# Optimization experiments

Hardware: AMD Instinct MI355X
Metric: run time of the kernel (lower is better)

The kernel has to match this reference:

```python
import jax, jax.numpy as jnp
import numpy as np
from jax import lax

K = 8            # number of object slots
H = 250          # hidden / fc_size
EPS = 1e-5
DN = ('NCHW', 'OIHW', 'NCHW')


def ln_all(x):
    # F.layer_norm over all non-batch dims, no affine params (torch init: w=1,b=0)
    ax = tuple(range(1, x.ndim))
    m = jnp.mean(x, ax, keepdims=True)
    v = jnp.var(x, ax, keepdims=True)
    return (x - m) * lax.rsqrt(v + EPS)


def ln_last(x):
    # nn.LayerNorm(feat) -> last dim only
    m = jnp.mean(x, -1, keepdims=True)
    v = jnp.var(x, -1, keepdims=True)
    return (x - m) * lax.rsqrt(v + EPS)


def conv(x, w, b):
    # torch Conv2d(k=4, s=2, p=1), NCHW
    y = lax.conv_general_dilated(x, w, (2, 2), [(1, 1), (1, 1)], dimension_numbers=DN)
    return y + b[None, :, None, None]


def up4(x):
    return jnp.repeat(jnp.repeat(x, 4, axis=2), 4, axis=3)


def setup_inputs():
    ks = jax.random.split(jax.random.key(0), 20)
    bk = 48 * K
    p = lambda i, shape, s: jax.random.normal(ks[i], shape, jnp.float32) * s
    z = lambda n: jnp.zeros((n,), jnp.float32)
    return dict(
        x=p(0, (bk, 4096), 1.0),
        state=p(1, (bk, H), 1.0),
        # encoder convs (OIHW) + fc
        c1w=p(2, (16, 1, 4, 4), 0.25), c1b=z(16),
        c2w=p(3, (32, 16, 4, 4), 0.06), c2b=z(32),
        c3w=p(4, (64, 32, 4, 4), 0.04), c3b=z(64),
        efc_w=p(5, (4096, 512), 0.016), efc_b=z(512),
        # R_NEM (weights stored as [in, out])
        renc_w=p(6, (H, H), 0.06), renc_b=z(H),
        core_w=p(7, (2 * H, H), 0.045), core_b=z(H),
        ctx_w=p(8, (H, H), 0.06), ctx_b=z(H),
        att1_w=p(9, (H, 100), 0.06), att1_b=z(100),
        att2_w=p(10, (100, 1), 0.1), att2_b=z(1),
        out_w=p(11, (2 * H + 512, H), 0.03), out_b=z(H),
        # decoder fcs + convs
        dfc1_w=p(12, (H, 512), 0.06), dfc1_b=z(512),
        dfc2_w=p(13, (512, 4096), 0.045), dfc2_b=z(4096),
        d1w=p(14, (32, 64, 4, 4), 0.03), d1b=z(32),
        d2w=p(15, (16, 32, 4, 4), 0.045), d2b=z(16),
        d3w=p(16, (1, 16, 4, 4), 0.06), d3b=z(1),
    )


def reference(x, state, c1w, c1b, c2w, c2b, c3w, c3b, efc_w, efc_b,
              renc_w, renc_b, core_w, core_b, ctx_w, ctx_b,
              att1_w, att1_b, att2_w, att2_b, out_w, out_b,
              dfc1_w, dfc1_b, dfc2_w, dfc2_b, d1w, d1b, d2w, d2b, d3w, d3b):
    bk = x.shape[0]
    b = bk // K

    # ---------------- EncoderLayer ----------------
    def inwrap(h, w, bias):  # InputWrapper conv branch: NHWC -> permute(0,3,2,1) -> conv -> back
        y = conv(jnp.transpose(h, (0, 3, 2, 1)), w, bias)
        return jax.nn.elu(ln_all(jnp.transpose(y, (0, 3, 2, 1))))

    h = x.reshape(bk, 64, 64, 1)
    h = inwrap(h, c1w, c1b)                 # (bk,32,32,16)
    h = inwrap(h, c2w, c2b)                 # (bk,16,16,32)
    h = inwrap(h, c3w, c3b)                 # (bk,8,8,64)
    h = h.reshape(bk, -1)                   # (bk,4096)
    h = jax.nn.elu(ln_last(h @ efc_w + efc_b))   # (bk,512)

    # ---------------- R_NEM (RecurrentLayer) ----------------
    s1 = jax.nn.relu(ln_last(state @ renc_w + renc_b))   # (bk,H)
    s1r = s1.reshape(b, K, H)
    idx = np.array([[j for j in range(K) if j != i] for i in range(K)])  # (K,K-1)
    cs = s1r[:, idx, :]                                    # context: (b,K,K-1,H)
    fs = jnp.broadcast_to(s1r[:, :, None, :], cs.shape)    # focus copies
    pair = jnp.concatenate([fs, cs], axis=-1)              # (b,K,K-1,2H)
    core = jax.nn.relu(ln_last(pair @ core_w + core_b))    # (b,K,K-1,H)
    ctx = jax.nn.relu(ln_last(core @ ctx_w + ctx_b))       # (b,K,K-1,H)
    att = jax.nn.sigmoid(jnp.tanh(ln_last(core @ att1_w + att1_b)) @ att2_w + att2_b)  # (b,K,K-1,1)
    effect = jnp.sum(ctx * att, axis=2).reshape(bk, H)     # attention-weighted sum over K-1
    total = jnp.concatenate([s1, effect, h], axis=1)       # (bk, 2H+512)
    new_state = total @ out_w + out_b                      # (bk,H)
    xr = jax.nn.sigmoid(ln_last(new_state))
    state_out = jax.nn.sigmoid(new_state)

    # ---------------- DecoderLayer ----------------
    d = jax.nn.relu(ln_last(xr @ dfc1_w + dfc1_b))         # (bk,512)
    d = jax.nn.relu(ln_last(d @ dfc2_w + dfc2_b))          # (bk,4096)
    d = d.reshape(bk, 8, 8, 64)

    def outwrap(t, w, bias):
        y = conv(up4(jnp.transpose(t, (0, 3, 2, 1))), w, bias)
        return jnp.transpose(y, (0, 3, 2, 1))

    d = jax.nn.relu(ln_all(outwrap(d, d1w, d1b)))          # (bk,16,16,32)
    d = jax.nn.relu(ln_all(outwrap(d, d2w, d2b)))          # (bk,32,32,16)
    d = jax.nn.sigmoid(outwrap(d, d3w, d3b))               # (bk,64,64,1), no LN
    x_out = d.reshape(bk, -1)                              # (bk,4096)
    return x_out, state_out
```

## Files before the change

kernel.cpp:

```cpp
#include <hip/hip_runtime.h>
#include <hip/hip_bf16.h>
#include <math.h>

#define ST_ENC2 0
#define ST_ENC3 1
#define ST_DEC1 2
#define ST_DEC2 3
#define ST_ENC1 4

typedef __attribute__((ext_vector_type(8))) short bf16x8;
typedef __attribute__((ext_vector_type(4))) float f32x4;

__device__ __forceinline__ float eluf(float v){ return v > 0.f ? v : expm1f(v); }
__device__ __forceinline__ float sigf(float v){ return 1.f/(1.f+expf(-v)); }
__device__ __forceinline__ unsigned short f2bf(float f){
  unsigned u = __float_as_uint(f);
  u += 0x7FFFu + ((u >> 16) & 1u);
  return (unsigned short)(u >> 16);
}
__device__ __forceinline__ float bf2f(short s){
  return __uint_as_float(((unsigned)(unsigned short)s) << 16);
}

__device__ __forceinline__ void block_reduce2(float& a, float& b, float* sbuf){
  __syncthreads();
  for (int off = 32; off; off >>= 1){
    a += __shfl_down(a, off);
    b += __shfl_down(b, off);
  }
  int lane = threadIdx.x & 63, w = threadIdx.x >> 6;
  if (lane == 0){ sbuf[2*w] = a; sbuf[2*w+1] = b; }
  __syncthreads();
  if (threadIdx.x == 0){
    int nw = blockDim.x >> 6;
    float sa = 0.f, sb = 0.f;
    for (int i = 0; i < nw; i++){ sa += sbuf[2*i]; sb += sbuf[2*i+1]; }
    sbuf[0] = sa; sbuf[1] = sb;
  }
  __syncthreads();
  a = sbuf[0]; b = sbuf[1];
}

__device__ __forceinline__ float fold_sum(const float* __restrict__ w, int O, int I,
                                          int o, int i, int pa, int pb, int da, int db){
  float s = 0.f;
  for (int kh = 0; kh < 4; kh++){
    bool inh = (pb==0) ? (db==0 ? (kh==0) : (kh>=1)) : (db==0 ? (kh<=2) : (kh==3));
    if (!inh) continue;
    for (int kw = 0; kw < 4; kw++){
      bool inw = (pa==0) ? (da==0 ? (kw==0) : (kw>=1)) : (da==0 ? (kw<=2) : (kw==3));
      if (!inw) continue;
      s += w[((o*I + i)*4 + kh)*4 + kw];
    }
  }
  return s;
}
__device__ __forceinline__ void fold_elem(const float* __restrict__ w, float* __restrict__ CW,
                                          int O, int I, int l){
  int o = l % O; int q = l / O;
  int da = q & 1, db = (q>>1)&1, pa = (q>>2)&1, pb = (q>>3)&1, i = q>>4;
  CW[(((pb*2+pa)*4 + db*2+da)*I + i)*O + o] = fold_sum(w, O, I, o, i, pa, pb, da, db);
}
__device__ __forceinline__ void cvtc2_elem(const float* __restrict__ w, short* __restrict__ D, int l){
  int i = l & 15, t = (l>>4) & 15, o = l>>8;
  D[l] = (short)f2bf(w[(o*16 + i)*16 + t]);
}
__device__ __forceinline__ void cvtc3_elem(const float* __restrict__ w, short* __restrict__ D, int l){
  int i = l & 31, t = (l>>5) & 15, o = l>>9;
  D[l] = (short)f2bf(w[(o*32 + i)*16 + t]);
}
__device__ __forceinline__ void foldd1_elem(const float* __restrict__ w, short* __restrict__ D, int l){
  int i = l & 63, tap = (l>>6)&3, o = (l>>8)&31, ph = l>>13;
  D[l] = (short)f2bf(fold_sum(w, 32, 64, o, i, ph&1, ph>>1, tap&1, tap>>1));
}
__device__ __forceinline__ void foldd2_elem(const float* __restrict__ w, short* __restrict__ D, int l){
  int i = l & 31, tap = (l>>5)&3, o = (l>>7)&15, ph = l>>11;
  D[l] = (short)f2bf(fold_sum(w, 16, 32, o, i, ph&1, ph>>1, tap&1, tap>>1));
}

__global__ __launch_bounds__(256) void prep_all(
  float* __restrict__ stat,
  const float* __restrict__ d3w, float* __restrict__ CWT3,
  const float* __restrict__ c2w, short* __restrict__ BtC2,
  const float* __restrict__ c3w, short* __restrict__ BtC3,
  const float* __restrict__ d1w, short* __restrict__ BD1,
  const float* __restrict__ d2w, short* __restrict__ BD2,
  const float* __restrict__ state, short* __restrict__ SBF)
{
  const int S0=3840, F3=S0+256, P2=F3+8192, P3=P2+32768, P4=P3+32768, P5=P4+8192,
            TOTAL=P5+98304;
  for (int l = blockIdx.x*blockDim.x + threadIdx.x; l < TOTAL; l += gridDim.x*blockDim.x){
    if (l < S0)      stat[l] = 0.f;
    else if (l < F3) fold_elem(d3w, CWT3, 1, 16, l - S0);
    else if (l < P2) cvtc2_elem(c2w, BtC2, l - F3);
    else if (l < P3) cvtc3_elem(c3w, BtC3, l - P2);
    else if (l < P4) foldd1_elem(d1w, BD1, l - P3);
    else if (l < P5) foldd2_elem(d2w, BD2, l - P4);
    else {
      int q = l - P5;
      int n = q >> 8, k = q & 255;
      SBF[q] = (k < 250) ? (short)f2bf(state[n*250 + k]) : (short)0;
    }
  }
}

__global__ __launch_bounds__(256) void transpose_cvt_all(
  const float* __restrict__ efc,  short* __restrict__ Defc,
  const float* __restrict__ dfc2, short* __restrict__ Ddfc2,
  const float* __restrict__ outw, short* __restrict__ Dout,
  const float* __restrict__ corew,short* __restrict__ Dcore,
  const float* __restrict__ dfc1, short* __restrict__ Ddfc1,
  const float* __restrict__ renc, short* __restrict__ Drenc,
  const float* __restrict__ ctx,  short* __restrict__ Dctx,
  const float* __restrict__ att1, short* __restrict__ Datt1)
{
  int bx = blockIdx.x;
  const float* W; short* D; int K, N, Kp, base;
  if      (bx < 512) { W=efc;  D=Defc;  K=4096; N=512;  Kp=4096; base=0;    }
  else if (bx < 1024){ W=dfc2; D=Ddfc2; K=512;  N=4096; Kp=512;  base=512;  }
  else if (bx < 1088){ W=outw; D=Dout;  K=1012; N=250;  Kp=1024; base=1024; }
  else if (bx < 1120){ W=corew;D=Dcore; K=500;  N=250;  Kp=512;  base=1088; }
  else if (bx < 1152){ W=dfc1; D=Ddfc1; K=250;  N=512;  Kp=256;  base=1120; }
  else if (bx < 1168){ W=renc; D=Drenc; K=250;  N=250;  Kp=256;  base=1152; }
  else if (bx < 1184){ W=ctx;  D=Dctx;  K=250;  N=250;  Kp=256;  base=1168; }
  else               { W=att1; D=Datt1; K=250;  N=100;  Kp=256;  base=1184; }
  int t = bx - base;
  int tpr = Kp >> 6;
  int tk = t % tpr, tn = t / tpr;
  __shared__ short tile[64][65];
  int c = threadIdx.x & 63, r4 = threadIdx.x >> 6;
  int n0 = tn*64, k0 = tk*64;
  #pragma unroll 4
  for (int p = 0; p < 16; p++){
    int r = r4*16 + p;
    int k = k0 + r, n = n0 + c;
    float v = (k < K && n < N) ? W[(size_t)k*N + n] : 0.f;
    tile[c][r] = (short)f2bf(v);
  }
  __syncthreads();
  #pragma unroll 4
  for (int p = 0; p < 16; p++){
    int nn = r4*16 + p;
    int n = n0 + nn;
    if (n < N) D[(size_t)n*Kp + k0 + c] = tile[nn][c];
  }
}

__global__ __launch_bounds__(256) void cvt_ln_elu(
    const short* __restrict__ inb, const float* __restrict__ stat, short* __restrict__ outb)
{
  int n = blockIdx.x, tid = threadIdx.x;
  float sm = stat[n*2], sq = stat[n*2+1];
  float m = sm*(1.f/4096.f), rs = rsqrtf(sq*(1.f/4096.f) - m*m + 1e-5f);
  const short* ip = inb + (size_t)n*4096;
  short* op = outb + (size_t)n*4096;
  for (int l = tid*4; l < 4096; l += 1024){
    uint2 rv = *(const uint2*)&ip[l];
    float v0 = bf2f((short)(rv.x & 0xFFFF)), v1 = bf2f((short)(rv.x >> 16));
    float v2 = bf2f((short)(rv.y & 0xFFFF)), v3 = bf2f((short)(rv.y >> 16));
    uint2 pk;
    pk.x = f2bf(eluf((v0-m)*rs)) | ((unsigned)f2bf(eluf((v1-m)*rs))<<16);
    pk.y = f2bf(eluf((v2-m)*rs)) | ((unsigned)f2bf(eluf((v3-m)*rs))<<16);
    *(uint2*)&op[l] = pk;
  }
}

__global__ __launch_bounds__(256) void gemm_mfma(
    const short* __restrict__ Ab, const short* __restrict__ Bt,
    float* __restrict__ P, int M, int N, int Kp, int Kc)
{
  __shared__ __align__(16) short As[64*32];
  __shared__ __align__(16) short Bs[64*32];
  int tid = threadIdx.x;
  int bm = blockIdx.y*64, bn = blockIdx.x*64;
  int kb = blockIdx.z * Kc;
  int kend = kb + Kc;

  int r = tid >> 2, c = tid & 3;
  const short* Arow = Ab + (size_t)(bm + r)*Kp;
  int gn = bn + r;
  bool bval = gn < N;
  const short* Brow = Bt + (size_t)gn*Kp;

  uint4 hA, hB;
  auto load_regs = [&](int k0){
    hA = *(const uint4*)&Arow[k0 + c*8];
    hB = bval ? *(const uint4*)&Brow[k0 + c*8] : make_uint4(0,0,0,0);
  };
  auto write_lds = [&](){
    *(uint4*)&As[r*32 + c*8] = hA;
    *(uint4*)&Bs[r*32 + c*8] = hB;
  };

  int wave = tid >> 6;
  int ln = tid & 15, quad = (tid >> 4) & 3;
  int wr = (wave >> 1) * 32, wc = (wave & 1) * 32;

  f32x4 zero = {0.f, 0.f, 0.f, 0.f};
  f32x4 acc[2][2] = {{zero, zero}, {zero, zero}};

  load_regs(kb);
  write_lds();
  __syncthreads();
  for (int k0 = kb; k0 < kend; k0 += 32){
    int nxt = k0 + 32;
    if (nxt < kend) load_regs(nxt);
    bf16x8 a0 = *(const bf16x8*)&As[(wr +      ln)*32 + quad*8];
    bf16x8 a1 = *(const bf16x8*)&As[(wr + 16 + ln)*32 + quad*8];
    bf16x8 b0 = *(const bf16x8*)&Bs[(wc +      ln)*32 + quad*8];
    bf16x8 b1 = *(const bf16x8*)&Bs[(wc + 16 + ln)*32 + quad*8];
    acc[0][0] = __builtin_amdgcn_mfma_f32_16x16x32_bf16(a0, b0, acc[0][0], 0, 0, 0);
    acc[0][1] = __builtin_amdgcn_mfma_f32_16x16x32_bf16(a0, b1, acc[0][1], 0, 0, 0);
    acc[1][0] = __builtin_amdgcn_mfma_f32_16x16x32_bf16(a1, b0, acc[1][0], 0, 0, 0);
    acc[1][1] = __builtin_amdgcn_mfma_f32_16x16x32_bf16(a1, b1, acc[1][1], 0, 0, 0);
    __syncthreads();
    if (nxt < kend){ write_lds(); __syncthreads(); }
  }

  float* Pout = P + (size_t)blockIdx.z*M*N;
  #pragma unroll
  for (int t = 0; t < 2; t++)
    #pragma unroll
    for (int u = 0; u < 2; u++)
      #pragma unroll
      for (int j = 0; j < 4; j++){
        int row = bm + wr + t*16 + quad*4 + j;
        int col = bn + wc + u*16 + ln;
        if (col < N) Pout[(size_t)row*N + col] = acc[t][u][j];
      }
}

__global__ __launch_bounds__(256) void reduce_ln(
    const float* __restrict__ Pp, const float* __restrict__ bias,
    void* __restrict__ outp, int M, int N, int KS, int os, int act, int obf)
{
  __shared__ float rowbuf[4096];
  __shared__ float sbuf[16];
  int row = blockIdx.x;
  size_t MN = (size_t)M*N;
  float s = 0.f, s2 = 0.f;
  for (int c = threadIdx.x; c < N; c += 256){
    float v = bias[c];
    for (int ks = 0; ks < KS; ks++) v += Pp[ks*MN + (size_t)row*N + c];
    rowbuf[c] = v; s += v; s2 += v*v;
  }
  block_reduce2(s, s2, sbuf);
  float m = s / N;
  float r = rsqrtf(s2/N - m*m + 1e-5f);
  for (int c = threadIdx.x; c < N; c += 256){
    float v = (rowbuf[c]-m)*r;
    if (act == 1) v = fmaxf(v, 0.f);
    else if (act == 2) v = eluf(v);
    else if (act == 3) v = tanhf(v);
    if (obf) ((short*)outp)[(size_t)row*os + c] = f2bf(v);
    else     ((float*)outp)[(size_t)row*os + c] = v;
  }
}

__global__ __launch_bounds__(256) void reduce_ns(
    const float* __restrict__ Pp, const float* __restrict__ bias,
    short* __restrict__ XRb, float* __restrict__ so, int M, int N, int KS)
{
  __shared__ float rowbuf[256];
  __shared__ float sbuf[16];
  int row = blockIdx.x;
  size_t MN = (size_t)M*N;
  float s = 0.f, s2 = 0.f;
  for (int c = threadIdx.x; c < N; c += 256){
    float v = bias[c];
    for (int ks = 0; ks < KS; ks++) v += Pp[ks*MN + (size_t)row*N + c];
    rowbuf[c] = v; s += v; s2 += v*v;
  }
  block_reduce2(s, s2, sbuf);
  float m = s / N;
  float r = rsqrtf(s2/N - m*m + 1e-5f);
  for (int c = threadIdx.x; c < N; c += 256){
    float v = rowbuf[c];
    XRb[(size_t)row*256 + c] = f2bf(sigf((v-m)*r));
    so[(size_t)row*N + c] = sigf(v);
  }
}

__global__ __launch_bounds__(256) void enc_conv1_ig(
    const float* __restrict__ x, const float* __restrict__ w, const float* __restrict__ bias,
    short* __restrict__ outp, float* __restrict__ stat)
{
  __shared__ __align__(16) float in_t[66*68];
  __shared__ float sbuf[16];
  int n = blockIdx.x, tid = threadIdx.x;
  for (int l = tid; l < 66*68; l += 256) in_t[l] = 0.f;
  __syncthreads();
  const float* xin = x + (size_t)n*4096;
  for (int l4 = tid; l4 < 1024; l4 += 256){
    float4 v = *(const float4*)&xin[l4*4];
    int aa = (l4*4) >> 6, bb = (l4*4) & 63;
    float* dst = &in_t[(aa+1)*68 + bb + 1];
    dst[0]=v.x; dst[1]=v.y; dst[2]=v.z; dst[3]=v.w;
  }
  int o = tid & 15;
  float wr[16];
  #pragma unroll
  for (int t = 0; t < 16; t++) wr[t] = w[o*16 + t];
  float bv = bias[o];
  __syncthreads();
  float s = 0.f, s2 = 0.f;
  short* op = outp + (size_t)n*16384;
  for (int r = 0; r < 64; r++){
    int idx = tid + (r<<8);
    int bq = (idx>>4)&31, aq = idx>>9;
    int a0 = 2*aq, b0 = 2*bq;
    float acc = bv;
    #pragma unroll
    for (int kw = 0; kw < 4; kw++){
      const float* row = &in_t[(a0+kw)*68 + b0];
      float2 p0 = *(const float2*)&row[0];
      float2 p1 = *(const float2*)&row[2];
      acc += p0.x*wr[0*4+kw] + p0.y*wr[1*4+kw] + p1.x*wr[2*4+kw] + p1.y*wr[3*4+kw];
    }
    op[idx] = f2bf(acc);
    s += acc; s2 += acc*acc;
  }
  block_reduce2(s, s2, sbuf);
  if (tid == 0){ atomicAdd(&stat[n*2], s); atomicAdd(&stat[n*2+1], s2); }
}

__global__ __launch_bounds__(256) void enc_conv2_mfma(
    const short* __restrict__ in, const short* __restrict__ Bt, const float* __restrict__ bias,
    const float* __restrict__ stat_in, short* __restrict__ outp, float* __restrict__ stat)
{
  __shared__ __align__(16) short in_t[34*34*16];
  __shared__ float sbuf[16];
  int n = blockIdx.x, tid = threadIdx.x;
  float smv = stat_in[n*2], sqv = stat_in[n*2+1];
  float m = smv*(1.f/16384.f), rs = rsqrtf(sqv*(1.f/16384.f) - m*m + 1e-5f);
  for (int l = tid; l < 34*34*16/4; l += 256) ((unsigned long long*)in_t)[l] = 0ull;
  __syncthreads();
  const short* ip = in + (size_t)n*16384;
  for (int l = tid; l < 4096; l += 256){
    int i4 = l & 3, bb = (l>>2) & 31, aa = l>>7;
    uint2 rv = *(const uint2*)&ip[aa*512 + bb*16 + i4*4];
    float v0 = bf2f((short)(rv.x & 0xFFFF)), v1 = bf2f((short)(rv.x >> 16));
    float v2 = bf2f((short)(rv.y & 0xFFFF)), v3 = bf2f((short)(rv.y >> 16));
    uint2 pk;
    pk.x = f2bf(eluf((v0-m)*rs)) | ((unsigned)f2bf(eluf((v1-m)*rs))<<16);
    pk.y = f2bf(eluf((v2-m)*rs)) | ((unsigned)f2bf(eluf((v3-m)*rs))<<16);
    *(uint2*)&in_t[((aa+1)*34 + (bb+1))*16 + i4*4] = pk;
  }
  int wave = tid>>6, ln = tid&15, quad = (tid>>4)&3;
  bf16x8 bfr[2][8];
  #pragma unroll
  for (int nt = 0; nt < 2; nt++){
    const short* Brow = Bt + (nt*16 + ln)*256;
    #pragma unroll
    for (int ks = 0; ks < 8; ks++)
      bfr[nt][ks] = *(const bf16x8*)&Brow[ks*32 + quad*8];
  }
  __syncthreads();
  f32x4 z = {0.f,0.f,0.f,0.f};
  f32x4 acc[2][4] = {{z,z,z,z},{z,z,z,z}};
  int tapq = quad>>1, io = (quad&1)*8;
  #pragma unroll
  for (int ks = 0; ks < 8; ks++){
    int t = 2*ks + tapq;
    int kh = t>>2, kw = t&3;
    #pragma unroll
    for (int mt = 0; mt < 4; mt++){
      int p = (wave*4 + mt)*16 + ln;
      int oa = p>>4, ob = p&15;
      bf16x8 a = *(const bf16x8*)&in_t[((2*oa+kw)*34 + (2*ob+kh))*16 + io];
      acc[0][mt] = __builtin_amdgcn_mfma_f32_16x16x32_bf16(a, bfr[0][ks], acc[0][mt],0,0,0);
      acc[1][mt] = __builtin_amdgcn_mfma_f32_16x16x32_bf16(a, bfr[1][ks], acc[1][mt],0,0,0);
    }
  }
  float s = 0.f, s2 = 0.f;
  short* op = outp + (size_t)n*8192;
  #pragma unroll
  for (int nt = 0; nt < 2; nt++){
    int o = nt*16 + ln;
    float bz = bias[o];
    #pragma unroll
    for (int mt = 0; mt < 4; mt++)
      #pragma unroll
      for (int j = 0; j < 4; j++){
        int p = (wave*4 + mt)*16 + quad*4 + j;
        float v = acc[nt][mt][j] + bz;
        s += v; s2 += v*v;
        int oa = p>>4, ob = p&15;
        op[oa*512 + ob*32 + o] = f2bf(v);
      }
  }
  block_reduce2(s, s2, sbuf);
  if (tid == 0){ atomicAdd(&stat[n*2], s); atomicAdd(&stat[n*2+1], s2); }
}

__global__ __launch_bounds__(256) void enc_conv3_mfma(
    const short* __restrict__ in, const short* __restrict__ Bt, const float* __restrict__ bias,
    const float* __restrict__ stat_in, short* __restrict__ outp, float* __restrict__ stat)
{
  __shared__ __align__(16) short in_t[18*18*32];
  __shared__ float sbuf[16];
  int n = blockIdx.x, tid = threadIdx.x;
  float smv = stat_in[n*2], sqv = stat_in[n*2+1];
  float m = smv*(1.f/8192.f), rs = rsqrtf(sqv*(1.f/8192.f) - m*m + 1e-5f);
  for (int l = tid; l < 18*18*32/4; l += 256) ((unsigned long long*)in_t)[l] = 0ull;
  __syncthreads();
  const short* ip = in + (size_t)n*8192;
  for (int l = tid; l < 2048; l += 256){
    int i4 = l & 7, bb = (l>>3)&15, aa = l>>7;
    uint2 rv = *(const uint2*)&ip[aa*512 + bb*32 + i4*4];
    float v0 = bf2f((short)(rv.x & 0xFFFF)), v1 = bf2f((short)(rv.x >> 16));
    float v2 = bf2f((short)(rv.y & 0xFFFF)), v3 = bf2f((short)(rv.y >> 16));
    uint2 pk;
    pk.x = f2bf(eluf((v0-m)*rs)) | ((unsigned)f2bf(eluf((v1-m)*rs))<<16);
    pk.y = f2bf(eluf((v2-m)*rs)) | ((unsigned)f2bf(eluf((v3-m)*rs))<<16);
    *(uint2*)&in_t[((aa+1)*18 + (bb+1))*32 + i4*4] = pk;
  }
  int wave = tid>>6, ln = tid&15, quad = (tid>>4)&3;
  int o = wave*16 + ln;
  bf16x8 bfr[16];
  {
    const short* Brow = Bt + o*512;
    #pragma unroll
    for (int ks = 0; ks < 16; ks++)
      bfr[ks] = *(const bf16x8*)&Brow[ks*32 + quad*8];
  }
  __syncthreads();
  f32x4 z = {0.f,0.f,0.f,0.f};
  f32x4 acc[4] = {z,z,z,z};
  #pragma unroll
  for (int ks = 0; ks < 16; ks++){
    int kh = ks>>2, kw = ks&3;
    #pragma unroll
    for (int mt = 0; mt < 4; mt++){
      int p = mt*16 + ln;
      int oa = p>>3, ob = p&7;
      bf16x8 a = *(const bf16x8*)&in_t[((2*oa+kw)*18 + (2*ob+kh))*32 + quad*8];
      acc[mt] = __builtin_amdgcn_mfma_f32_16x16x32_bf16(a, bfr[ks], acc[mt],0,0,0);
    }
  }
  float s = 0.f, s2 = 0.f;
  float bz = bias[o];
  short* op = outp + (size_t)n*4096;
  #pragma unroll
  for (int mt = 0; mt < 4; mt++)
    #pragma unroll
    for (int j = 0; j < 4; j++){
      int p = mt*16 + quad*4 + j;
      int oa = p>>3, ob = p&7;
      float v = acc[mt][j] + bz;
      s += v; s2 += v*v;
      op[oa*512 + ob*64 + o] = f2bf(v);
    }
  block_reduce2(s, s2, sbuf);
  if (tid == 0){ atomicAdd(&stat[n*2], s); atomicAdd(&stat[n*2+1], s2); }
}

__global__ __launch_bounds__(256) void dec_conv1_mfma(
    const short* __restrict__ in, const short* __restrict__ Bd, const float* __restrict__ bias,
    short* __restrict__ outp, float* __restrict__ stat)
{
  __shared__ __align__(16) short in_t[10*10*64];
  __shared__ float sbuf[16];
  int n = blockIdx.x, tid = threadIdx.x;
  for (int l = tid; l < 10*10*64/4; l += 256) ((unsigned long long*)in_t)[l] = 0ull;
  __syncthreads();
  const short* ip = in + (size_t)n*4096;
  for (int l = tid; l < 1024; l += 256){
    int i4 = l & 15, sb = (l>>4)&7, sa = l>>7;
    *(uint2*)&in_t[((sa+1)*10 + (sb+1))*64 + i4*4] = *(const uint2*)&ip[sa*512 + sb*64 + i4*4];
  }
  int wave = tid>>6, ln = tid&15, quad = (tid>>4)&3;
  int pa = wave & 1, pb = wave >> 1;
  bf16x8 bfr[2][8];
  #pragma unroll
  for (int nt = 0; nt < 2; nt++){
    const short* Brow = Bd + (wave*32 + nt*16 + ln)*256;
    #pragma unroll
    for (int ks = 0; ks < 8; ks++)
      bfr[nt][ks] = *(const bf16x8*)&Brow[ks*32 + quad*8];
  }
  __syncthreads();
  f32x4 z = {0.f,0.f,0.f,0.f};
  f32x4 acc[2][4] = {{z,z,z,z},{z,z,z,z}};
  #pragma unroll
  for (int ks = 0; ks < 8; ks++){
    int tap = ks>>1, ibase = (ks&1)*32 + quad*8;
    int da = tap & 1, db = tap >> 1;
    #pragma unroll
    for (int mt = 0; mt < 4; mt++){
      int p = mt*16 + ln;
      int ta = p>>3, tb = p&7;
      bf16x8 a = *(const bf16x8*)&in_t[((ta+da+pa)*10 + (tb+db+pb))*64 + ibase];
      acc[0][mt] = __builtin_amdgcn_mfma_f32_16x16x32_bf16(a, bfr[0][ks], acc[0][mt],0,0,0);
      acc[1][mt] = __builtin_amdgcn_mfma_f32_16x16x32_bf16(a, bfr[1][ks], acc[1][mt],0,0,0);
    }
  }
  float s = 0.f, s2 = 0.f;
  short* op = outp + (size_t)n*8192;
  #pragma unroll
  for (int nt = 0; nt < 2; nt++){
    int o = nt*16 + ln;
    float bz = bias[o];
    #pragma unroll
    for (int mt = 0; mt < 4; mt++)
      #pragma unroll
      for (int j = 0; j < 4; j++){
        int p = mt*16 + quad*4 + j;
        int ta = p>>3, tb = p&7;
        float v = acc[nt][mt][j] + bz;
        s += v; s2 += v*v;
        op[(2*ta+pa)*512 + (2*tb+pb)*32 + o] = f2bf(v);
      }
  }
  block_reduce2(s, s2, sbuf);
  if (tid == 0){ atomicAdd(&stat[n*2], s); atomicAdd(&stat[n*2+1], s2); }
}

__global__ __launch_bounds__(256) void dec_conv2_mfma(
    const short* __restrict__ in, const short* __restrict__ Bd, const float* __restrict__ bias,
    const float* __restrict__ stat_in, short* __restrict__ outp, float* __restrict__ stat)
{
  __shared__ __align__(16) short in_t[18*18*32];
  __shared__ float sbuf[16];
  int n = blockIdx.x, tid = threadIdx.x;
  float smv = stat_in[n*2], sqv = stat_in[n*2+1];
  float m = smv*(1.f/8192.f), rs = rsqrtf(sqv*(1.f/8192.f) - m*m + 1e-5f);
  for (int l = tid; l < 18*18*32/4; l += 256) ((unsigned long long*)in_t)[l] = 0ull;
  __syncthreads();
  const short* ip = in + (size_t)n*8192;
  for (int l = tid; l < 2048; l += 256){
    int i4 = l & 7, sb = (l>>3)&15, sa = l>>7;
    uint2 rv = *(const uint2*)&ip[sa*512 + sb*32 + i4*4];
    float v0 = bf2f((short)(rv.x & 0xFFFF)), v1 = bf2f((short)(rv.x >> 16));
    float v2 = bf2f((short)(rv.y & 0xFFFF)), v3 = bf2f((short)(rv.y >> 16));
    uint2 pk;
    pk.x = f2bf(fmaxf((v0-m)*rs,0.f)) | ((unsigned)f2bf(fmaxf((v1-m)*rs,0.f))<<16);
    pk.y = f2bf(fmaxf((v2-m)*rs,0.f)) | ((unsigned)f2bf(fmaxf((v3-m)*rs,0.f))<<16);
    *(uint2*)&in_t[((sa+1)*18 + (sb+1))*32 + i4*4] = pk;
  }
  int wave = tid>>6, ln = tid&15, quad = (tid>>4)&3;
  int pa = wave & 1, pb = wave >> 1;
  bf16x8 bfr[4];
  {
    const short* Brow = Bd + (wave*16 + ln)*128;
    #pragma unroll
    for (int ks = 0; ks < 4; ks++)
      bfr[ks] = *(const bf16x8*)&Brow[ks*32 + quad*8];
  }
  __syncthreads();
  f32x4 z = {0.f,0.f,0.f,0.f};
  f32x4 acc[16] = {z,z,z,z,z,z,z,z,z,z,z,z,z,z,z,z};
  #pragma unroll
  for (int ks = 0; ks < 4; ks++){
    int da = ks & 1, db = ks >> 1;
    #pragma unroll
    for (int mt = 0; mt < 16; mt++){
      int p = mt*16 + ln;
      int ta = p>>4, tb = p&15;
      bf16x8 a = *(const bf16x8*)&in_t[((ta+da+pa)*18 + (tb+db+pb))*32 + quad*8];
      acc[mt] = __builtin_amdgcn_mfma_f32_16x16x32_bf16(a, bfr[ks], acc[mt],0,0,0);
    }
  }
  float s = 0.f, s2 = 0.f;
  float bz = bias[ln];
  short* op = outp + (size_t)n*16384;
  #pragma unroll
  for (int mt = 0; mt < 16; mt++)
    #pragma unroll
    for (int j = 0; j < 4; j++){
      int p = mt*16 + quad*4 + j;
      int ta = p>>4, tb = p&15;
      float v = acc[mt][j] + bz;
      s += v; s2 += v*v;
      op[(2*ta+pa)*512 + (2*tb+pb)*16 + ln] = f2bf(v);
    }
  block_reduce2(s, s2, sbuf);
  if (tid == 0){ atomicAdd(&stat[n*2], s); atomicAdd(&stat[n*2+1], s2); }
}

__global__ __launch_bounds__(256) void dec_conv3_ig(
    const short* __restrict__ in, const float* __restrict__ CWT, const float* __restrict__ bias,
    const float* __restrict__ stat_in, float* __restrict__ outp)
{
  __shared__ __align__(16) float in_t[9792];
  __shared__ __align__(16) float wl[256];
  int bx = blockIdx.x;
  int n = bx >> 1, b0 = (bx & 1) * 32, tb0 = b0 >> 1;
  int tid = threadIdx.x;
  float sm = stat_in[n*2], sq = stat_in[n*2+1];
  float m = sm*(1.f/16384.f), rs = rsqrtf(sq*(1.f/16384.f) - m*m + 1e-5f);
  const short* ip = in + (size_t)n*16384;
  for (int l = tid; l < 9792; l += 256){
    int i = l & 15, sb = (l >> 4) % 18, sap = l / 288;
    int sa = sap - 1, sbg = tb0 - 1 + sb;
    float v = 0.f;
    if ((unsigned)sa < 32u && (unsigned)sbg < 32u)
      v = fmaxf((bf2f(ip[sa*512 + sbg*16 + i])-m)*rs, 0.f);
    in_t[(sap*18 + sb)*16 + i] = v;
  }
  for (int l = tid; l < 256; l += 256) wl[l] = CWT[l];
  __syncthreads();
  float bv = bias[0];
  int bl = tid & 31, ath = tid >> 5;
  int b = b0 + bl;
  int tb = b >> 1, pb = b & 1;
  float* op = outp + (size_t)n*4096;
  #pragma unroll
  for (int j = 0; j < 8; j++){
    int a = ath*8 + j;
    int ta = a >> 1, pa = a & 1;
    float4 s4 = make_float4(0.f,0.f,0.f,0.f);
    #pragma unroll
    for (int db = 0; db < 2; db++){
      int sb = tb + db + (pb ? 0 : -1);
      int sbl = sb - (tb0 - 1);
      #pragma unroll
      for (int da = 0; da < 2; da++){
        int sa = ta + da + (pa ? 0 : -1);
        int sap = sa + 1;
        const float4* A4 = (const float4*)&in_t[(sap*18 + sbl)*16];
        const float4* B4 = (const float4*)&wl[((pb*2+pa)*4 + db*2+da)*16];
        #pragma unroll
        for (int q = 0; q < 4; q++){
          float4 av = A4[q], bw = B4[q];
          s4.x += av.x*bw.x; s4.y += av.y*bw.y;
          s4.z += av.z*bw.z; s4.w += av.w*bw.w;
        }
      }
    }
    op[a*64 + b] = sigf(bv + s4.x + s4.y + s4.z + s4.w);
  }
}

__global__ __launch_bounds__(256) void pair_build(const short* __restrict__ tot, short* __restrict__ P)
{
  int r = blockIdx.x;
  int jj = r % 7, fi = r / 7;
  int i = fi & 7, j = fi >> 3;
  int jidx = jj < i ? jj : jj+1;
  const short* srcf = tot + (size_t)fi*1024;
  const short* srco = tot + (size_t)(j*8+jidx)*1024;
  short* op = P + (size_t)r*512;
  for (int c = threadIdx.x; c < 250; c += blockDim.x){
    op[c] = srcf[c];
    op[250+c] = srco[c];
  }
  if (threadIdx.x < 12) op[500 + threadIdx.x] = 0;
}

__global__ __launch_bounds__(256) void effect_kernel(const float* __restrict__ X1,
    const float* __restrict__ A1, const float* __restrict__ w2, const float* __restrict__ b2,
    short* __restrict__ tot)
{
  __shared__ float att_s[8];
  int row = blockIdx.x, tid = threadIdx.x;
  int jj = tid >> 5, l = tid & 31;
  float d = 0.f;
  if (jj < 7){
    const float* ip = A1 + ((size_t)row*7 + jj)*100;
    for (int c = l; c < 100; c += 32) d += ip[c]*w2[c];
  }
  for (int off = 16; off; off >>= 1) d += __shfl_down(d, off, 32);
  if (jj < 7 && l == 0) att_s[jj] = sigf(d + b2[0]);
  __syncthreads();
  for (int h = tid; h < 250; h += 256){
    float s = 0.f;
    #pragma unroll
    for (int q = 0; q < 7; q++)
      s += X1[((size_t)row*7+q)*250 + h] * att_s[q];
    tot[(size_t)row*1024 + 250 + h] = f2bf(s);
  }
}

extern "C" void kernel_launch(void* const* d_in, const int* in_sizes, int n_in,
                              void* d_out, int out_size, void* d_ws, size_t ws_size,
                              hipStream_t stream) {
  const float* x      = (const float*)d_in[0];
  const float* state  = (const float*)d_in[1];
  const float* c1w    = (const float*)d_in[2];
  const float* c1b    = (const float*)d_in[3];
  const float* c2w    = (const float*)d_in[4];
  const float* c2b    = (const float*)d_in[5];
  const float* c3w    = (const float*)d_in[6];
  const float* c3b    = (const float*)d_in[7];
  const float* efc_w  = (const float*)d_in[8];
  const float* efc_b  = (const float*)d_in[9];
  const float* renc_w = (const float*)d_in[10];
  const float* renc_b = (const float*)d_in[11];
  const float* core_w = (const float*)d_in[12];
  const float* core_b = (const float*)d_in[13];
  const float* ctx_w  = (const float*)d_in[14];
  const float* ctx_b  = (const float*)d_in[15];
  const float* att1_w = (const float*)d_in[16];
  const float* att1_b = (const float*)d_in[17];
  const float* att2_w = (const float*)d_in[18];
  const float* att2_b = (const float*)d_in[19];
  const float* out_w  = (const float*)d_in[20];
  const float* out_b  = (const float*)d_in[21];
  const float* dfc1_w = (const float*)d_in[22];
  const float* dfc1_b = (const float*)d_in[23];
  const float* dfc2_w = (const float*)d_in[24];
  const float* dfc2_b = (const float*)d_in[25];
  const float* d1w    = (const float*)d_in[26];
  const float* d1b    = (const float*)d_in[27];
  const float* d2w    = (const float*)d_in[28];
  const float* d2b    = (const float*)d_in[29];
  const float* d3w    = (const float*)d_in[30];
  const float* d3b    = (const float*)d_in[31];

  float* wsf = (float*)d_ws;
  size_t o = 0;
  float* PB  = wsf + o; o += (size_t)1600*1024;
  float* X1  = wsf + o; o += (size_t)2688*250;
  float* A1  = wsf + o; o += (size_t)2688*100;
  float* CWT3 = wsf + o; o += 256;
  float* STAT = wsf + o; o += 5*384*2;
  short* E1b  = (short*)(wsf + o); o += (size_t)384*16384/2;
  short* E2b  = (short*)(wsf + o); o += (size_t)384*8192/2;
  short* E3b  = (short*)(wsf + o); o += (size_t)384*4096/2;
  short* TOTb = (short*)(wsf + o); o += (size_t)384*1024/2;
  short* Prb  = (short*)(wsf + o); o += (size_t)2688*512/2;
  short* C1b  = (short*)(wsf + o); o += (size_t)2688*256/2;
  short* XRb  = (short*)(wsf + o); o += (size_t)384*256/2;
  short* G1b  = (short*)(wsf + o); o += (size_t)384*512/2;
  short* ECV  = (short*)(wsf + o); o += (size_t)384*4096/2;
  short* SBF  = (short*)(wsf + o); o += (size_t)384*256/2;
  short* BtC2 = (short*)(wsf + o); o += 8192/2;
  short* BtC3 = (short*)(wsf + o); o += 32768/2;
  short* BD1  = (short*)(wsf + o); o += 32768/2;
  short* BD2  = (short*)(wsf + o); o += 8192/2;
  short* BT_efc  = (short*)(wsf + o); o += 2097152/2;
  short* BT_renc = (short*)(wsf + o); o += 64000/2;
  short* BT_core = (short*)(wsf + o); o += 128000/2;
  short* BT_ctx  = (short*)(wsf + o); o += 64000/2;
  short* BT_att1 = (short*)(wsf + o); o += 25600/2;
  short* BT_out  = (short*)(wsf + o); o += 256000/2;
  short* BT_dfc1 = (short*)(wsf + o); o += 131072/2;
  short* BT_dfc2 = (short*)(wsf + o); o += 2097152/2;
  short* D1b = E2b;
  short* D2b = E1b;
  short* G2b = E3b;

  float* xout = (float*)d_out;
  float* sout = xout + (size_t)384*4096;

  prep_all<<<256, 256, 0, stream>>>(STAT,
      d3w, CWT3, c2w, BtC2, c3w, BtC3, d1w, BD1, d2w, BD2, state, SBF);
  transpose_cvt_all<<<1192, 256, 0, stream>>>(
      efc_w, BT_efc, dfc2_w, BT_dfc2, out_w, BT_out, core_w, BT_core,
      dfc1_w, BT_dfc1, renc_w, BT_renc, ctx_w, BT_ctx, att1_w, BT_att1);

  enc_conv1_ig<<<384, 256, 0, stream>>>(x, c1w, c1b, E1b, STAT + ST_ENC1*768);
  enc_conv2_mfma<<<384, 256, 0, stream>>>(E1b, BtC2, c2b, STAT + ST_ENC1*768, E2b, STAT + ST_ENC2*768);
  enc_conv3_mfma<<<384, 256, 0, stream>>>(E2b, BtC3, c3b, STAT + ST_ENC2*768, E3b, STAT + ST_ENC3*768);
  cvt_ln_elu<<<384, 256, 0, stream>>>(E3b, STAT + ST_ENC3*768, ECV);
  gemm_mfma<<<dim3(8,6,8), 256, 0, stream>>>(ECV, BT_efc, PB, 384, 512, 4096, 512);
  reduce_ln<<<384, 256, 0, stream>>>(PB, efc_b, TOTb+500, 384, 512, 8, 1024, 2, 1);

  gemm_mfma<<<dim3(4,6,8), 256, 0, stream>>>(SBF, BT_renc, PB, 384, 250, 256, 32);
  reduce_ln<<<384, 256, 0, stream>>>(PB, renc_b, TOTb, 384, 250, 8, 1024, 1, 1);
  pair_build<<<2688, 256, 0, stream>>>(TOTb, Prb);
  gemm_mfma<<<dim3(4,42,2), 256, 0, stream>>>(Prb, BT_core, PB, 2688, 250, 512, 256);
  reduce_ln<<<2688, 256, 0, stream>>>(PB, core_b, C1b, 2688, 250, 2, 256, 1, 1);
  gemm_mfma<<<dim3(4,42,2), 256, 0, stream>>>(C1b, BT_ctx, PB, 2688, 250, 256, 128);
  reduce_ln<<<2688, 256, 0, stream>>>(PB, ctx_b, X1, 2688, 250, 2, 250, 1, 0);
  gemm_mfma<<<dim3(2,42,4), 256, 0, stream>>>(C1b, BT_att1, PB, 2688, 100, 256, 64);
  reduce_ln<<<2688, 256, 0, stream>>>(PB, att1_b, A1, 2688, 100, 4, 100, 3, 0);
  effect_kernel<<<384, 256, 0, stream>>>(X1, A1, att2_w, att2_b, TOTb);

  gemm_mfma<<<dim3(4,6,8), 256, 0, stream>>>(TOTb, BT_out, PB, 384, 250, 1024, 128);
  reduce_ns<<<384, 256, 0, stream>>>(PB, out_b, XRb, sout, 384, 250, 8);

  gemm_mfma<<<dim3(8,6,4), 256, 0, stream>>>(XRb, BT_dfc1, PB, 384, 512, 256, 64);
  reduce_ln<<<384, 256, 0, stream>>>(PB, dfc1_b, G1b, 384, 512, 4, 512, 1, 1);
  gemm_mfma<<<dim3(64,6,1), 256, 0, stream>>>(G1b, BT_dfc2, PB, 384, 4096, 512, 512);
  reduce_ln<<<384, 256, 0, stream>>>(PB, dfc2_b, G2b, 384, 4096, 1, 4096, 1, 1);

  dec_conv1_mfma<<<384, 256, 0, stream>>>(G2b, BD1, d1b, D1b, STAT + ST_DEC1*768);
  dec_conv2_mfma<<<384, 256, 0, stream>>>(D1b, BD2, d2b, STAT + ST_DEC1*768, D2b, STAT + ST_DEC2*768);
  dec_conv3_ig<<<768, 256, 0, stream>>>(D2b, CWT3, d3b, STAT + ST_DEC2*768, xout);

  (void)in_sizes; (void)n_in; (void)out_size; (void)ws_size;
}
```

Baseline: 353.3 us.

## Fuse pair-building into core GEMM, merge prep kernels, fuse ctx/att/effect epilogues

The core GEMM now gathers its own and the other object's rows from TOTb, so the 2688-row pair matrix is no longer materialized. To make that possible, TOTb is re-laid out with 256-aligned segments, and the weight transposes insert zero rows to match the padded K. The two prep kernels are merged into one launch. The ctx LayerNorm, attention LayerNorm, tanh, dot and sigmoid, and the effect sum are fused into a single per-object kernel that reads the GEMM partials directly, which removes several launches and intermediate buffers. The cost is serial per-row block reductions inside the fused kernel, which uses only 384 blocks.

```diff
diff --git a/kernel.cpp b/kernel.cpp
--- a/kernel.cpp
+++ b/kernel.cpp
@@ -78,33 +78,7 @@
   D[l] = (short)f2bf(fold_sum(w, 16, 32, o, i, ph&1, ph>>1, tap&1, tap>>1));
 }
 
-__global__ __launch_bounds__(256) void prep_all(
-  float* __restrict__ stat,
-  const float* __restrict__ d3w, float* __restrict__ CWT3,
-  const float* __restrict__ c2w, short* __restrict__ BtC2,
-  const float* __restrict__ c3w, short* __restrict__ BtC3,
-  const float* __restrict__ d1w, short* __restrict__ BD1,
-  const float* __restrict__ d2w, short* __restrict__ BD2,
-  const float* __restrict__ state, short* __restrict__ SBF)
-{
-  const int S0=3840, F3=S0+256, P2=F3+8192, P3=P2+32768, P4=P3+32768, P5=P4+8192,
-            TOTAL=P5+98304;
-  for (int l = blockIdx.x*blockDim.x + threadIdx.x; l < TOTAL; l += gridDim.x*blockDim.x){
-    if (l < S0)      stat[l] = 0.f;
-    else if (l < F3) fold_elem(d3w, CWT3, 1, 16, l - S0);
-    else if (l < P2) cvtc2_elem(c2w, BtC2, l - F3);
-    else if (l < P3) cvtc3_elem(c3w, BtC3, l - P2);
-    else if (l < P4) foldd1_elem(d1w, BD1, l - P3);
-    else if (l < P5) foldd2_elem(d2w, BD2, l - P4);
-    else {
-      int q = l - P5;
-      int n = q >> 8, k = q & 255;
-      SBF[q] = (k < 250) ? (short)f2bf(state[n*250 + k]) : (short)0;
-    }
-  }
-}
-
-__global__ __launch_bounds__(256) void transpose_cvt_all(
+__global__ __launch_bounds__(256) void prep_combined(
   const float* __restrict__ efc,  short* __restrict__ Defc,
   const float* __restrict__ dfc2, short* __restrict__ Ddfc2,
   const float* __restrict__ outw, short* __restrict__ Dout,
@@ -112,14 +86,45 @@
   const float* __restrict__ dfc1, short* __restrict__ Ddfc1,
   const float* __restrict__ renc, short* __restrict__ Drenc,
   const float* __restrict__ ctx,  short* __restrict__ Dctx,
-  const float* __restrict__ att1, short* __restrict__ Datt1)
+  const float* __restrict__ att1, short* __restrict__ Datt1,
+  float* __restrict__ stat,
+  const float* __restrict__ d3w, float* __restrict__ CWT3,
+  const float* __restrict__ c2w, short* __restrict__ BtC2,
+  const float* __restrict__ c3w, short* __restrict__ BtC3,
+  const float* __restrict__ d1w, short* __restrict__ BD1,
+  const float* __restrict__ d2w, short* __restrict__ BD2,
+  const float* __restrict__ state, short* __restrict__ SBF,
+  short* __restrict__ TOTb)
 {
   int bx = blockIdx.x;
-  const float* W; short* D; int K, N, Kp, base;
+  if (bx >= 1192){
+    const int S0=3840, F3=S0+256, P2=F3+8192, P3=P2+32768, P4=P3+32768, P5=P4+8192,
+              ST=P5+98304, TOTAL=ST+4608;
+    for (int l = (bx-1192)*256 + threadIdx.x; l < TOTAL; l += 256*256){
+      if (l < S0)      stat[l] = 0.f;
+      else if (l < F3) fold_elem(d3w, CWT3, 1, 16, l - S0);
+      else if (l < P2) cvtc2_elem(c2w, BtC2, l - F3);
+      else if (l < P3) cvtc3_elem(c3w, BtC3, l - P2);
+      else if (l < P4) foldd1_elem(d1w, BD1, l - P3);
+      else if (l < P5) foldd2_elem(d2w, BD2, l - P4);
+      else if (l < ST){
+        int q = l - P5;
+        int n = q >> 8, k = q & 255;
+        SBF[q] = (k < 250) ? (short)f2bf(state[n*250 + k]) : (short)0;
+      } else {
+        int q = l - ST;
+        int row = q / 12, cc = q % 12;
+        int col = cc < 6 ? 250 + cc : 506 + (cc - 6);
+        TOTb[row*1024 + col] = 0;
+      }
+    }
+    return;
+  }
+  const float* W; short* D; int K, N, Kp, base, mode = 0;
   if      (bx < 512) { W=efc;  D=Defc;  K=4096; N=512;  Kp=4096; base=0;    }
   else if (bx < 1024){ W=dfc2; D=Ddfc2; K=512;  N=4096; Kp=512;  base=512;  }
-  else if (bx < 1088){ W=outw; D=Dout;  K=1012; N=250;  Kp=1024; base=1024; }
-  else if (bx < 1120){ W=corew;D=Dcore; K=500;  N=250;  Kp=512;  base=1088; }
+  else if (bx < 1088){ W=outw; D=Dout;  K=1012; N=250;  Kp=1024; base=1024; mode=2; }
+  else if (bx < 1120){ W=corew;D=Dcore; K=500;  N=250;  Kp=512;  base=1088; mode=1; }
   else if (bx < 1152){ W=dfc1; D=Ddfc1; K=250;  N=512;  Kp=256;  base=1120; }
   else if (bx < 1168){ W=renc; D=Drenc; K=250;  N=250;  Kp=256;  base=1152; }
   else if (bx < 1184){ W=ctx;  D=Dctx;  K=250;  N=250;  Kp=256;  base=1168; }
@@ -134,7 +139,12 @@
   for (int p = 0; p < 16; p++){
     int r = r4*16 + p;
     int k = k0 + r, n = n0 + c;
-    float v = (k < K && n < N) ? W[(size_t)k*N + n] : 0.f;
+    int ksrc = k; bool valid;
+    if (mode == 0) valid = (k < K);
+    else if (mode == 1){ valid = (k < 250) || (k >= 256 && k < 506); ksrc = k < 256 ? k : k - 6; }
+    else { valid = (k < 250) || (k >= 256 && k < 506) || (k >= 512);
+           ksrc = k < 256 ? k : (k < 512 ? k - 6 : k - 12); }
+    float v = (valid && n < N) ? W[(size_t)ksrc*N + n] : 0.f;
     tile[c][r] = (short)f2bf(v);
   }
   __syncthreads();
@@ -230,6 +240,78 @@
       }
 }
 
+__global__ __launch_bounds__(256) void gemm_core_mfma(
+    const short* __restrict__ Tb, const short* __restrict__ Bt,
+    float* __restrict__ P, int M, int N, int Kc)
+{
+  __shared__ __align__(16) short As[64*32];
+  __shared__ __align__(16) short Bs[64*32];
+  int tid = threadIdx.x;
+  int bm = blockIdx.y*64, bn = blockIdx.x*64;
+  int kb = blockIdx.z * Kc;
+  int kend = kb + Kc;
+
+  int r = tid >> 2, c = tid & 3;
+  int gr = bm + r;
+  int jj2 = gr % 7, fi2 = gr / 7;
+  int ii = fi2 & 7, j2 = fi2 >> 3;
+  int jidx = jj2 < ii ? jj2 : jj2 + 1;
+  const short* own = Tb + (size_t)fi2*1024;
+  const short* oth = Tb + (size_t)(j2*8 + jidx)*1024;
+  int gn = bn + r;
+  bool bval = gn < N;
+  const short* Brow = Bt + (size_t)gn*512;
+
+  uint4 hA, hB;
+  auto load_regs = [&](int k0){
+    int kk = k0 + c*8;
+    const short* src = (kk & 256) ? oth : own;
+    hA = *(const uint4*)&src[kk & 255];
+    hB = bval ? *(const uint4*)&Brow[kk] : make_uint4(0,0,0,0);
+  };
+  auto write_lds = [&](){
+    *(uint4*)&As[r*32 + c*8] = hA;
+    *(uint4*)&Bs[r*32 + c*8] = hB;
+  };
+
+  int wave = tid >> 6;
+  int ln = tid & 15, quad = (tid >> 4) & 3;
+  int wr = (wave >> 1) * 32, wc = (wave & 1) * 32;
+
+  f32x4 zero = {0.f, 0.f, 0.f, 0.f};
+  f32x4 acc[2][2] = {{zero, zero}, {zero, zero}};
+
+  load_regs(kb);
+  write_lds();
+  __syncthreads();
+  for (int k0 = kb; k0 < kend; k0 += 32){
+    int nxt = k0 + 32;
+    if (nxt < kend) load_regs(nxt);
+    bf16x8 a0 = *(const bf16x8*)&As[(wr +      ln)*32 + quad*8];
+    bf16x8 a1 = *(const bf16x8*)&As[(wr + 16 + ln)*32 + quad*8];
+    bf16x8 b0 = *(const bf16x8*)&Bs[(wc +      ln)*32 + quad*8];
+    bf16x8 b1 = *(const bf16x8*)&Bs[(wc + 16 + ln)*32 + quad*8];
+    acc[0][0] = __builtin_amdgcn_mfma_f32_16x16x32_bf16(a0, b0, acc[0][0], 0, 0, 0);
+    acc[0][1] = __builtin_amdgcn_mfma_f32_16x16x32_bf16(a0, b1, acc[0][1], 0, 0, 0);
+    acc[1][0] = __builtin_amdgcn_mfma_f32_16x16x32_bf16(a1, b0, acc[1][0], 0, 0, 0);
+    acc[1][1] = __builtin_amdgcn_mfma_f32_16x16x32_bf16(a1, b1, acc[1][1], 0, 0, 0);
+    __syncthreads();
+    if (nxt < kend){ write_lds(); __syncthreads(); }
+  }
+
+  float* Pout = P + (size_t)blockIdx.z*M*N;
+  #pragma unroll
+  for (int t = 0; t < 2; t++)
+    #pragma unroll
+    for (int u = 0; u < 2; u++)
+      #pragma unroll
+      for (int j = 0; j < 4; j++){
+        int row = bm + wr + t*16 + quad*4 + j;
+        int col = bn + wc + u*16 + ln;
+        if (col < N) Pout[(size_t)row*N + col] = acc[t][u][j];
+      }
+}
+
 __global__ __launch_bounds__(256) void reduce_ln(
     const float* __restrict__ Pp, const float* __restrict__ bias,
     void* __restrict__ outp, int M, int N, int KS, int os, int act, int obf)
@@ -278,6 +360,52 @@
     float v = rowbuf[c];
     XRb[(size_t)row*256 + c] = f2bf(sigf((v-m)*r));
     so[(size_t)row*N + c] = sigf(v);
+  }
+}
+
+__global__ __launch_bounds__(256) void ctx_att_effect(
+    const float* __restrict__ Pc, const float* __restrict__ ctx_b,
+    const float* __restrict__ Pa, const float* __restrict__ att1_b,
+    const float* __restrict__ w2, const float* __restrict__ b2,
+    short* __restrict__ tot)
+{
+  __shared__ float ctxs[7][256];
+  __shared__ float att_s[8];
+  __shared__ float sbuf[16];
+  int fi = blockIdx.x, tid = threadIdx.x;
+  const size_t MN = (size_t)2688*250, MN2 = (size_t)2688*100;
+  for (int jj = 0; jj < 7; jj++){
+    int row = fi*7 + jj;
+    float s = 0.f, s2 = 0.f, v = 0.f;
+    if (tid < 250){
+      v = ctx_b[tid] + Pc[(size_t)row*250 + tid] + Pc[MN + (size_t)row*250 + tid];
+      s = v; s2 = v*v;
+    }
+    block_reduce2(s, s2, sbuf);
+    float m = s*(1.f/250.f);
+    float r = rsqrtf(s2*(1.f/250.f) - m*m + 1e-5f);
+    if (tid < 250) ctxs[jj][tid] = fmaxf((v-m)*r, 0.f);
+    float va = 0.f; s = 0.f; s2 = 0.f;
+    if (tid < 100){
+      va = att1_b[tid];
+      #pragma unroll
+      for (int ks = 0; ks < 4; ks++) va += Pa[ks*MN2 + (size_t)row*100 + tid];
+      s = va; s2 = va*va;
+    }
+    block_reduce2(s, s2, sbuf);
+    m = s*0.01f;
+    r = rsqrtf(s2*0.01f - m*m + 1e-5f);
+    float d = (tid < 100) ? tanhf((va-m)*r)*w2[tid] : 0.f;
+    float dummy = 0.f;
+    block_reduce2(d, dummy, sbuf);
+    if (tid == 0) att_s[jj] = sigf(d + b2[0]);
+  }
+  __syncthreads();
+  if (tid < 250){
+    float s = 0.f;
+    #pragma unroll
+    for (int q = 0; q < 7; q++) s += ctxs[q][tid]*att_s[q];
+    tot[(size_t)fi*1024 + 256 + tid] = f2bf(s);
   }
 }
 
@@ -629,46 +757,6 @@
       }
     }
     op[a*64 + b] = sigf(bv + s4.x + s4.y + s4.z + s4.w);
-  }
-}
-
-__global__ __launch_bounds__(256) void pair_build(const short* __restrict__ tot, short* __restrict__ P)
-{
-  int r = blockIdx.x;
-  int jj = r % 7, fi = r / 7;
-  int i = fi & 7, j = fi >> 3;
-  int jidx = jj < i ? jj : jj+1;
-  const short* srcf = tot + (size_t)fi*1024;
-  const short* srco = tot + (size_t)(j*8+jidx)*1024;
-  short* op = P + (size_t)r*512;
-  for (int c = threadIdx.x; c < 250; c += blockDim.x){
-    op[c] = srcf[c];
-    op[250+c] = srco[c];
-  }
-  if (threadIdx.x < 12) op[500 + threadIdx.x] = 0;
-}
-
-__global__ __launch_bounds__(256) void effect_kernel(const float* __restrict__ X1,
-    const float* __restrict__ A1, const float* __restrict__ w2, const float* __restrict__ b2,
-    short* __restrict__ tot)
-{
-  __shared__ float att_s[8];
-  int row = blockIdx.x, tid = threadIdx.x;
-  int jj = tid >> 5, l = tid & 31;
-  float d = 0.f;
-  if (jj < 7){
-    const float* ip = A1 + ((size_t)row*7 + jj)*100;
-    for (int c = l; c < 100; c += 32) d += ip[c]*w2[c];
-  }
-  for (int off = 16; off; off >>= 1) d += __shfl_down(d, off, 32);
-  if (jj < 7 && l == 0) att_s[jj] = sigf(d + b2[0]);
-  __syncthreads();
-  for (int h = tid; h < 250; h += 256){
-    float s = 0.f;
-    #pragma unroll
-    for (int q = 0; q < 7; q++)
-      s += X1[((size_t)row*7+q)*250 + h] * att_s[q];
-    tot[(size_t)row*1024 + 250 + h] = f2bf(s);
   }
 }
 
@@ -710,16 +798,14 @@
 
   float* wsf = (float*)d_ws;
   size_t o = 0;
-  float* PB  = wsf + o; o += (size_t)1600*1024;
-  float* X1  = wsf + o; o += (size_t)2688*250;
-  float* A1  = wsf + o; o += (size_t)2688*100;
+  float* PB   = wsf + o; o += (size_t)1600*1024;
+  float* PB2  = wsf + o; o += (size_t)2688*100*4;
   float* CWT3 = wsf + o; o += 256;
   float* STAT = wsf + o; o += 5*384*2;
   short* E1b  = (short*)(wsf + o); o += (size_t)384*16384/2;
   short* E2b  = (short*)(wsf + o); o += (size_t)384*8192/2;
   short* E3b  = (short*)(wsf + o); o += (size_t)384*4096/2;
   short* TOTb = (short*)(wsf + o); o += (size_t)384*1024/2;
-  short* Prb  = (short*)(wsf + o); o += (size_t)2688*512/2;
   short* C1b  = (short*)(wsf + o); o += (size_t)2688*256/2;
   short* XRb  = (short*)(wsf + o); o += (size_t)384*256/2;
   short* G1b  = (short*)(wsf + o); o += (size_t)384*512/2;
@@ -744,29 +830,25 @@
   float* xout = (float*)d_out;
   float* sout = xout + (size_t)384*4096;
 
-  prep_all<<<256, 256, 0, stream>>>(STAT,
-      d3w, CWT3, c2w, BtC2, c3w, BtC3, d1w, BD1, d2w, BD2, state, SBF);
-  transpose_cvt_all<<<1192, 256, 0, stream>>>(
+  prep_combined<<<1448, 256, 0, stream>>>(
       efc_w, BT_efc, dfc2_w, BT_dfc2, out_w, BT_out, core_w, BT_core,
-      dfc1_w, BT_dfc1, renc_w, BT_renc, ctx_w, BT_ctx, att1_w, BT_att1);
+      dfc1_w, BT_dfc1, renc_w, BT_renc, ctx_w, BT_ctx, att1_w, BT_att1,
+      STAT, d3w, CWT3, c2w, BtC2, c3w, BtC3, d1w, BD1, d2w, BD2, state, SBF, TOTb);
 
   enc_conv1_ig<<<384, 256, 0, stream>>>(x, c1w, c1b, E1b, STAT + ST_ENC1*768);
   enc_conv2_mfma<<<384, 256, 0, stream>>>(E1b, BtC2, c2b, STAT + ST_ENC1*768, E2b, STAT + ST_ENC2*768);
   enc_conv3_mfma<<<384, 256, 0, stream>>>(E2b, BtC3, c3b, STAT + ST_ENC2*768, E3b, STAT + ST_ENC3*768);
   cvt_ln_elu<<<384, 256, 0, stream>>>(E3b, STAT + ST_ENC3*768, ECV);
   gemm_mfma<<<dim3(8,6,8), 256, 0, stream>>>(ECV, BT_efc, PB, 384, 512, 4096, 512);
-  reduce_ln<<<384, 256, 0, stream>>>(PB, efc_b, TOTb+500, 384, 512, 8, 1024, 2, 1);
+  reduce_ln<<<384, 256, 0, stream>>>(PB, efc_b, TOTb+512, 384, 512, 8, 1024, 2, 1);
 
   gemm_mfma<<<dim3(4,6,8), 256, 0, stream>>>(SBF, BT_renc, PB, 384, 250, 256, 32);
   reduce_ln<<<384, 256, 0, stream>>>(PB, renc_b, TOTb, 384, 250, 8, 1024, 1, 1);
-  pair_build<<<2688, 256, 0, stream>>>(TOTb, Prb);
-  gemm_mfma<<<dim3(4,42,2), 256, 0, stream>>>(Prb, BT_core, PB, 2688, 250, 512, 256);
+  gemm_core_mfma<<<dim3(4,42,2), 256, 0, stream>>>(TOTb, BT_core, PB, 2688, 250, 256);
   reduce_ln<<<2688, 256, 0, stream>>>(PB, core_b, C1b, 2688, 250, 2, 256, 1, 1);
   gemm_mfma<<<dim3(4,42,2), 256, 0, stream>>>(C1b, BT_ctx, PB, 2688, 250, 256, 128);
-  reduce_ln<<<2688, 256, 0, stream>>>(PB, ctx_b, X1, 2688, 250, 2, 250, 1, 0);
-  gemm_mfma<<<dim3(2,42,4), 256, 0, stream>>>(C1b, BT_att1, PB, 2688, 100, 256, 64);
-  reduce_ln<<<2688, 256, 0, stream>>>(PB, att1_b, A1, 2688, 100, 4, 100, 3, 0);
-  effect_kernel<<<384, 256, 0, stream>>>(X1, A1, att2_w, att2_b, TOTb);
+  gemm_mfma<<<dim3(2,42,4), 256, 0, stream>>>(C1b, BT_att1, PB2, 2688, 100, 256, 64);
+  ctx_att_effect<<<384, 256, 0, stream>>>(PB, ctx_b, PB2, att1_b, att2_w, att2_b, TOTb);
 
   gemm_mfma<<<dim3(4,6,8), 256, 0, stream>>>(TOTb, BT_out, PB, 384, 250, 1024, 128);
   reduce_ns<<<384, 256, 0, stream>>>(PB, out_b, XRb, sout, 384, 250, 8);
```

Result: no change. 356.4 us (+0.9%).
